# Kernel optimization log

Hardware: AMD Instinct MI355X
Metric: run time of the kernel (lower is better)

Reference implementation:

```python
import jax, jax.numpy as jnp
import numpy as np

N = 100000
E = 1600000
IN_DIM = 128
HID_DIM = 128
OUT_DIM = 128


def _sage_conv(x, src, dst, W_l, b_l, W_r, num_nodes):
    """PyG SAGEConv with mean aggregation:
       out = mean_{j in N(i)} x_j @ W_l + b_l + x_i @ W_r
    edge_index convention: messages flow src -> dst."""
    msg = x[src]                                        # [E, d_in] gather
    agg_sum = jax.ops.segment_sum(msg, dst, num_segments=num_nodes)   # [N, d_in]
    cnt = jax.ops.segment_sum(jnp.ones((msg.shape[0],), x.dtype), dst,
                              num_segments=num_nodes)   # [N]
    agg = agg_sum / jnp.maximum(cnt, 1.0)[:, None]      # scatter-mean (0 for isolated nodes)
    return agg @ W_l + b_l + x @ W_r


def setup_inputs() -> dict:
    key = jax.random.key(0)
    ks = jax.random.split(key, 8)
    def glorot(k, fan_in, fan_out):
        s = jnp.sqrt(2.0 / (fan_in + fan_out))
        return jax.random.normal(k, (fan_in, fan_out), dtype=jnp.float32) * s
    x = jax.random.normal(ks[0], (N, IN_DIM), dtype=jnp.float32)
    edge_index = jax.random.randint(ks[1], (2, E), 0, N, dtype=jnp.int64)
    return {
        "x": x,
        "edge_index": edge_index,
        "W1_l": glorot(ks[2], IN_DIM, HID_DIM),
        "b1": jnp.zeros((HID_DIM,), jnp.float32),
        "W1_r": glorot(ks[3], IN_DIM, HID_DIM),
        "W2_l": glorot(ks[4], HID_DIM, OUT_DIM),
        "b2": jnp.zeros((OUT_DIM,), jnp.float32),
        "W2_r": glorot(ks[5], HID_DIM, OUT_DIM),
    }


def reference(x, edge_index, W1_l, b1, W1_r, W2_l, b2, W2_r):
    src, dst = edge_index[0], edge_index[1]
    h = _sage_conv(x, src, dst, W1_l, b1, W1_r, N)
    h = jax.nn.relu(h)
    # F.dropout(p=0.5, training=self.training): identity in eval mode
    out = _sage_conv(h, src, dst, W2_l, b2, W2_r, N)
    return out
```

## Files before the change

### kernel.cpp

```cpp
#include <hip/hip_runtime.h>
#include <hip/hip_bf16.h>

#define N_NODES 100000
#define N_EDGES 1600000
#define DIM 128
#define BR 32
#define ESTG 2048
#define NB 782
#define CHUNK 16384

typedef __attribute__((ext_vector_type(8))) short bf16x8;
typedef __attribute__((ext_vector_type(4))) float f32x4;
typedef __attribute__((ext_vector_type(2))) float f32x2;

#define OFF_ROWPTR 0
#define OFF_BCNT   (N_NODES + 4)
#define OFF_BBASE  (OFF_BCNT + NB)
#define OFF_BCUR   (OFF_BBASE + NB)
#define OFF_PAIRS  (OFF_BCUR + NB)
#define OFF_COLSRC (OFF_PAIRS + N_EDGES)
#define OFF_HB     (OFF_COLSRC + N_EDGES)
#define OFF_HF8    (OFF_HB + N_NODES * DIM / 2)
#define OFF_WB     (OFF_HF8 + N_NODES * DIM / 4)

__device__ inline unsigned int f2bf(float f) {
    unsigned int u = __float_as_uint(f);
    return (u + 0x7FFFu + ((u >> 16) & 1u)) >> 16;
}

__global__ __launch_bounds__(256) void conv_pack_kernel(
    const float* __restrict__ x, unsigned char* __restrict__ xf8,
    const float* __restrict__ W1l, const float* __restrict__ W1r,
    const float* __restrict__ W2l, const float* __restrict__ W2r,
    unsigned short* __restrict__ WB)
{
    const int b = blockIdx.x;
    const int tid = threadIdx.x;
    if (b < 6250) {
        long i = (long)(b * 256 + tid) * 8;
        float4 a = *(const float4*)(x + i);
        float4 c = *(const float4*)(x + i + 4);
        unsigned int w0 = 0, w1 = 0;
        w0 = __builtin_amdgcn_cvt_pk_fp8_f32(a.x, a.y, w0, false);
        w0 = __builtin_amdgcn_cvt_pk_fp8_f32(a.z, a.w, w0, true);
        w1 = __builtin_amdgcn_cvt_pk_fp8_f32(c.x, c.y, w1, false);
        w1 = __builtin_amdgcn_cvt_pk_fp8_f32(c.z, c.w, w1, true);
        uint2 o; o.x = w0; o.y = w1;
        *(uint2*)(xf8 + i) = o;
    } else {
        int t = (b - 6250) * 256 + tid;
        int layer = t >> 15;
        int rest  = t & 32767;
        int half  = rest >> 14;
        int idx   = rest & 16383;
        int k = idx >> 7;
        int n = idx & 127;
        const float* W = layer ? (half ? W2r : W2l) : (half ? W1r : W1l);
        int kk = half * 128 + k;
        WB[layer * 32768 + (((kk >> 3) * 128 + n) << 3) + (kk & 7)] =
            (unsigned short)f2bf(W[idx]);
    }
}

__global__ __launch_bounds__(256) void bhist_kernel(
    const int* __restrict__ dst, int* __restrict__ bcnt)
{
    __shared__ int histL[NB];
    const int tid = threadIdx.x;
    const int e0 = blockIdx.x * CHUNK;
    const int e1 = min(e0 + CHUNK, N_EDGES);
    for (int b = tid; b < NB; b += 256) histL[b] = 0;
    __syncthreads();
    for (int i = e0 + tid; i < e1; i += 256)
        atomicAdd(&histL[dst[i] >> 7], 1);
    __syncthreads();
    for (int b = tid; b < NB; b += 256) {
        int c = histL[b];
        if (c) atomicAdd(&bcnt[b], c);
    }
}

__global__ __launch_bounds__(1024) void bscan_kernel(
    const int* __restrict__ bcnt, int* __restrict__ bbase,
    int* __restrict__ bcur, int* __restrict__ rowptr)
{
    __shared__ int tmp[1024];
    int tid = threadIdx.x;
    int v = (tid < NB) ? bcnt[tid] : 0;
    tmp[tid] = v;
    __syncthreads();
    for (int off = 1; off < 1024; off <<= 1) {
        int t = (tid >= off) ? tmp[tid - off] : 0;
        __syncthreads();
        tmp[tid] += t;
        __syncthreads();
    }
    if (tid < NB) { int b = tmp[tid] - v; bbase[tid] = b; bcur[tid] = b; }
    if (tid == 0) rowptr[N_NODES] = N_EDGES;
}

__global__ __launch_bounds__(256) void bfill_kernel(
    const int* __restrict__ src, const int* __restrict__ dst,
    int* __restrict__ bcur, unsigned int* __restrict__ pairs)
{
    __shared__ int histL[NB];
    __shared__ int baseL[NB];
    const int tid = threadIdx.x;
    const int e0 = blockIdx.x * CHUNK;
    const int e1 = min(e0 + CHUNK, N_EDGES);
    for (int b = tid; b < NB; b += 256) histL[b] = 0;
    __syncthreads();
    for (int i = e0 + tid; i < e1; i += 256)
        atomicAdd(&histL[dst[i] >> 7], 1);
    __syncthreads();
    for (int b = tid; b < NB; b += 256) {
        int c = histL[b];
        baseL[b] = c ? atomicAdd(&bcur[b], c) : 0;
        histL[b] = 0;
    }
    __syncthreads();
    for (int i = e0 + tid; i < e1; i += 256) {
        int s = src[i];
        int d = dst[i];
        int bk = d >> 7;
        int r = atomicAdd(&histL[bk], 1);
        pairs[baseL[bk] + r] = (unsigned int)s | ((unsigned int)(d & 127) << 25);
    }
}

__global__ __launch_bounds__(256) void bucket_csr_kernel(
    const unsigned int* __restrict__ pairs,
    const int* __restrict__ bcnt, const int* __restrict__ bbase,
    int* __restrict__ rowptr, int* __restrict__ colsrc)
{
    __shared__ int histA[128], exclS[128], hist2[128];
    const int bucket = blockIdx.x;
    const int tid = threadIdx.x;
    const int cnt  = bcnt[bucket];
    const int base = bbase[bucket];
    if (tid < 128) { histA[tid] = 0; hist2[tid] = 0; }
    __syncthreads();
    for (int i = tid; i < cnt; i += 256)
        atomicAdd(&histA[pairs[base + i] >> 25], 1);
    __syncthreads();
    int v = 0;
    if (tid < 128) { v = histA[tid]; exclS[tid] = v; }
    __syncthreads();
    for (int off = 1; off < 128; off <<= 1) {
        int t = 0;
        if (tid < 128 && tid >= off) t = exclS[tid - off];
        __syncthreads();
        if (tid < 128) exclS[tid] += t;
        __syncthreads();
    }
    if (tid < 128) exclS[tid] -= v;
    const int node0 = bucket * 128;
    if (tid < 128 && node0 + tid < N_NODES)
        rowptr[node0 + tid] = base + exclS[tid];
    __syncthreads();
    for (int i = tid; i < cnt; i += 256) {
        unsigned int p = pairs[base + i];
        int dl = (int)(p >> 25);
        int r = atomicAdd(&hist2[dl], 1);
        colsrc[base + exclS[dl] + r] = (int)(p & 0x1FFFFFFu);
    }
}

__device__ inline void addfp8(float* acc, uint2 v) {
    f32x2 p;
    p = __builtin_amdgcn_cvt_pk_f32_fp8((int)v.x, false); acc[0] += p.x; acc[1] += p.y;
    p = __builtin_amdgcn_cvt_pk_f32_fp8((int)v.x, true);  acc[2] += p.x; acc[3] += p.y;
    p = __builtin_amdgcn_cvt_pk_f32_fp8((int)v.y, false); acc[4] += p.x; acc[5] += p.y;
    p = __builtin_amdgcn_cvt_pk_f32_fp8((int)v.y, true);  acc[6] += p.x; acc[7] += p.y;
}

__global__ __launch_bounds__(256, 5) void fused_sage_kernel(
    const unsigned char* __restrict__ f8,
    const float* __restrict__ selfF,
    const unsigned short* __restrict__ selfB,
    const int* __restrict__ rowptr,
    const int* __restrict__ colsrc,
    const unsigned short* __restrict__ WB,
    const float* __restrict__ bias,
    unsigned short* __restrict__ outb,
    unsigned char* __restrict__ outf8,
    float* __restrict__ outf,
    int mode)
{
    __shared__ unsigned short catS[BR * 256];
    __shared__ int eS[ESTG];

    const int tid = threadIdx.x;
    const int block_row = blockIdx.x * BR;
    const int ebase = rowptr[block_row];
    const int span  = rowptr[block_row + BR] - ebase;
    const int smax  = span < ESTG ? span : ESTG;

    for (int i = tid; i < smax; i += 256)
        eS[i] = colsrc[ebase + i] << 7;
    __syncthreads();

    const int c   = tid & 15;
    const int c8  = c * 8;
    const int grp = tid >> 4;

    #pragma unroll
    for (int it = 0; it < 2; ++it) {
        const int nl = grp * 2 + it;
        const int node = block_row + nl;
        const int s  = rowptr[node] - ebase;
        const int e_ = rowptr[node + 1] - ebase;
        const int lim = e_ < ESTG ? e_ : ESTG;

        uint4 sv;
        if (mode) {
            float4 sa = *(const float4*)(selfF + ((long)node << 7) + c8);
            float4 sb = *(const float4*)(selfF + ((long)node << 7) + c8 + 4);
            sv.x = f2bf(sa.x) | (f2bf(sa.y) << 16);
            sv.y = f2bf(sa.z) | (f2bf(sa.w) << 16);
            sv.z = f2bf(sb.x) | (f2bf(sb.y) << 16);
            sv.w = f2bf(sb.z) | (f2bf(sb.w) << 16);
        } else {
            sv = *(const uint4*)(selfB + ((long)node << 7) + c8);
        }

        float acc[8];
        #pragma unroll
        for (int q = 0; q < 8; ++q) acc[q] = 0.0f;

        int i = s;
        for (; i + 8 <= lim; i += 8) {
            const uint2 v0 = *(const uint2*)(f8 + eS[i + 0] + c8);
            const uint2 v1 = *(const uint2*)(f8 + eS[i + 1] + c8);
            const uint2 v2 = *(const uint2*)(f8 + eS[i + 2] + c8);
            const uint2 v3 = *(const uint2*)(f8 + eS[i + 3] + c8);
            const uint2 v4 = *(const uint2*)(f8 + eS[i + 4] + c8);
            const uint2 v5 = *(const uint2*)(f8 + eS[i + 5] + c8);
            const uint2 v6 = *(const uint2*)(f8 + eS[i + 6] + c8);
            const uint2 v7 = *(const uint2*)(f8 + eS[i + 7] + c8);
            addfp8(acc, v0); addfp8(acc, v1); addfp8(acc, v2); addfp8(acc, v3);
            addfp8(acc, v4); addfp8(acc, v5); addfp8(acc, v6); addfp8(acc, v7);
        }
        for (; i < lim; ++i) {
            const uint2 v = *(const uint2*)(f8 + eS[i] + c8);
            addfp8(acc, v);
        }
        for (; i < e_; ++i) {
            const uint2 v = *(const uint2*)(f8 + ((long)colsrc[ebase + i] << 7) + c8);
            addfp8(acc, v);
        }

        const float inv = 1.0f / fmaxf((float)(e_ - s), 1.0f);
        uint4 pv;
        pv.x = f2bf(acc[0] * inv) | (f2bf(acc[1] * inv) << 16);
        pv.y = f2bf(acc[2] * inv) | (f2bf(acc[3] * inv) << 16);
        pv.z = f2bf(acc[4] * inv) | (f2bf(acc[5] * inv) << 16);
        pv.w = f2bf(acc[6] * inv) | (f2bf(acc[7] * inv) << 16);
        const int sw = c ^ (nl & 7);
        *(uint4*)&catS[nl * 256 + sw * 8] = pv;
        *(uint4*)&catS[nl * 256 + 128 + sw * 8] = sv;
    }
    __syncthreads();

    const int w    = tid >> 6;
    const int l    = tid & 63;
    const int wm   = w & 1;
    const int wn   = w >> 1;
    const int lrow = l & 15;
    const int kgrp = l >> 4;
    const int ar   = wm * 16 + lrow;

    f32x4 acc4[4];
    #pragma unroll
    for (int t = 0; t < 4; ++t) acc4[t] = (f32x4){0.f, 0.f, 0.f, 0.f};

    #pragma unroll
    for (int step = 0; step < 8; ++step) {
        const int slot = step * 4 + kgrp;
        bf16x8 a = *(const bf16x8*)&catS[ar * 256 + ((slot ^ (ar & 7)) << 3)];
        #pragma unroll
        for (int t = 0; t < 4; ++t) {
            const int n = wn * 64 + t * 16 + lrow;
            bf16x8 b = *(const bf16x8*)(WB + ((slot * 128 + n) << 3));
            acc4[t] = __builtin_amdgcn_mfma_f32_16x16x32_bf16(a, b, acc4[t], 0, 0, 0);
        }
    }

    const long orow0 = block_row + wm * 16 + kgrp * 4;
    const int  cbase = wn * 64 + lrow;
    #pragma unroll
    for (int t = 0; t < 4; ++t) {
        const int col = cbase + t * 16;
        const float bb = bias[col];
        #pragma unroll
        for (int j = 0; j < 4; ++j) {
            float v = acc4[t][j] + bb;
            const long row = orow0 + j;
            if (mode) {
                v = fmaxf(v, 0.0f);
                outb[row * DIM + col] = (unsigned short)f2bf(v);
                outf8[row * DIM + col] =
                    (unsigned char)(__builtin_amdgcn_cvt_pk_fp8_f32(v, v, 0u, false) & 0xFFu);
            } else {
                outf[row * DIM + col] = v;
            }
        }
    }
}

extern "C" void kernel_launch(void* const* d_in, const int* in_sizes, int n_in,
                              void* d_out, int out_size, void* d_ws, size_t ws_size,
                              hipStream_t stream)
{
    const float* x   = (const float*)d_in[0];
    const int*   ei  = (const int*)d_in[1];
    const float* W1l = (const float*)d_in[2];
    const float* b1  = (const float*)d_in[3];
    const float* W1r = (const float*)d_in[4];
    const float* W2l = (const float*)d_in[5];
    const float* b2  = (const float*)d_in[6];
    const float* W2r = (const float*)d_in[7];
    float* out = (float*)d_out;

    const int* src = ei;
    const int* dst = ei + N_EDGES;

    int* wsi = (int*)d_ws;
    int* rowptr = wsi + OFF_ROWPTR;
    int* bcnt   = wsi + OFF_BCNT;
    int* bbase  = wsi + OFF_BBASE;
    int* bcur   = wsi + OFF_BCUR;
    unsigned int* pairs = (unsigned int*)(wsi + OFF_PAIRS);
    int* colsrc = wsi + OFF_COLSRC;
    unsigned short* hb  = (unsigned short*)(wsi + OFF_HB);
    unsigned char*  hf8 = (unsigned char*)(wsi + OFF_HF8);
    unsigned short* WB  = (unsigned short*)(wsi + OFF_WB);

    unsigned char* xf8 = (unsigned char*)d_out;

    hipMemsetAsync(bcnt, 0, (size_t)NB * sizeof(int), stream);

    conv_pack_kernel<<<6506, 256, 0, stream>>>(x, xf8, W1l, W1r, W2l, W2r, WB);

    const int eblocks = (N_EDGES + CHUNK - 1) / CHUNK;
    bhist_kernel<<<eblocks, 256, 0, stream>>>(dst, bcnt);
    bscan_kernel<<<1, 1024, 0, stream>>>(bcnt, bbase, bcur, rowptr);
    bfill_kernel<<<eblocks, 256, 0, stream>>>(src, dst, bcur, pairs);
    bucket_csr_kernel<<<NB, 256, 0, stream>>>(pairs, bcnt, bbase, rowptr, colsrc);

    const int gblocks = N_NODES / BR;
    fused_sage_kernel<<<gblocks, 256, 0, stream>>>(
        xf8, x, (const unsigned short*)nullptr, rowptr, colsrc,
        WB, b1, hb, hf8, (float*)nullptr, 1);
    fused_sage_kernel<<<gblocks, 256, 0, stream>>>(
        hf8, (const float*)nullptr, hb, rowptr, colsrc,
        WB + 32768, b2, (unsigned short*)nullptr, (unsigned char*)nullptr, out, 0);
}
```

Before: 216.7 us.

## Merge histogram into pack kernel, raise occupancy, and unroll gather tail

Folds the bucket-histogram kernel into the conversion/pack kernel as extra blocks, which removes one launch and lets the histogram overlap with the fp8 conversion. The fused SAGE kernel's minimum-waves hint goes from 5 to 8 and the shared edge staging buffer shrinks from 2048 to 1024 entries, aiming for more resident blocks. Edges beyond the stage then fall back to slower global colsrc reads. The scalar remainder loop becomes a 4/2/1 unrolled tail to expose more memory-level parallelism. The higher occupancy target may also force register spills.

```diff
diff --git a/kernel.cpp b/kernel.cpp
--- a/kernel.cpp
+++ b/kernel.cpp
@@ -5,7 +5,7 @@
 #define N_EDGES 1600000
 #define DIM 128
 #define BR 32
-#define ESTG 2048
+#define ESTG 1024
 #define NB 782
 #define CHUNK 16384
 
@@ -32,8 +32,10 @@
     const float* __restrict__ x, unsigned char* __restrict__ xf8,
     const float* __restrict__ W1l, const float* __restrict__ W1r,
     const float* __restrict__ W2l, const float* __restrict__ W2r,
-    unsigned short* __restrict__ WB)
-{
+    unsigned short* __restrict__ WB,
+    const int* __restrict__ dst, int* __restrict__ bcnt)
+{
+    __shared__ int histL[NB];
     const int b = blockIdx.x;
     const int tid = threadIdx.x;
     if (b < 6250) {
@@ -47,7 +49,7 @@
         w1 = __builtin_amdgcn_cvt_pk_fp8_f32(c.z, c.w, w1, true);
         uint2 o; o.x = w0; o.y = w1;
         *(uint2*)(xf8 + i) = o;
-    } else {
+    } else if (b < 6506) {
         int t = (b - 6250) * 256 + tid;
         int layer = t >> 15;
         int rest  = t & 32767;
@@ -59,24 +61,18 @@
         int kk = half * 128 + k;
         WB[layer * 32768 + (((kk >> 3) * 128 + n) << 3) + (kk & 7)] =
             (unsigned short)f2bf(W[idx]);
-    }
-}
-
-__global__ __launch_bounds__(256) void bhist_kernel(
-    const int* __restrict__ dst, int* __restrict__ bcnt)
-{
-    __shared__ int histL[NB];
-    const int tid = threadIdx.x;
-    const int e0 = blockIdx.x * CHUNK;
-    const int e1 = min(e0 + CHUNK, N_EDGES);
-    for (int b = tid; b < NB; b += 256) histL[b] = 0;
-    __syncthreads();
-    for (int i = e0 + tid; i < e1; i += 256)
-        atomicAdd(&histL[dst[i] >> 7], 1);
-    __syncthreads();
-    for (int b = tid; b < NB; b += 256) {
-        int c = histL[b];
-        if (c) atomicAdd(&bcnt[b], c);
+    } else {
+        const int e0 = (b - 6506) * CHUNK;
+        const int e1 = min(e0 + CHUNK, N_EDGES);
+        for (int q = tid; q < NB; q += 256) histL[q] = 0;
+        __syncthreads();
+        for (int i = e0 + tid; i < e1; i += 256)
+            atomicAdd(&histL[dst[i] >> 7], 1);
+        __syncthreads();
+        for (int q = tid; q < NB; q += 256) {
+            int c = histL[q];
+            if (c) atomicAdd(&bcnt[q], c);
+        }
     }
 }
 
@@ -174,7 +170,7 @@
     p = __builtin_amdgcn_cvt_pk_f32_fp8((int)v.y, true);  acc[6] += p.x; acc[7] += p.y;
 }
 
-__global__ __launch_bounds__(256, 5) void fused_sage_kernel(
+__global__ __launch_bounds__(256, 8) void fused_sage_kernel(
     const unsigned char* __restrict__ f8,
     const float* __restrict__ selfF,
     const unsigned short* __restrict__ selfB,
@@ -241,9 +237,24 @@
             addfp8(acc, v0); addfp8(acc, v1); addfp8(acc, v2); addfp8(acc, v3);
             addfp8(acc, v4); addfp8(acc, v5); addfp8(acc, v6); addfp8(acc, v7);
         }
-        for (; i < lim; ++i) {
+        if (i + 4 <= lim) {
+            const uint2 v0 = *(const uint2*)(f8 + eS[i + 0] + c8);
+            const uint2 v1 = *(const uint2*)(f8 + eS[i + 1] + c8);
+            const uint2 v2 = *(const uint2*)(f8 + eS[i + 2] + c8);
+            const uint2 v3 = *(const uint2*)(f8 + eS[i + 3] + c8);
+            addfp8(acc, v0); addfp8(acc, v1); addfp8(acc, v2); addfp8(acc, v3);
+            i += 4;
+        }
+        if (i + 2 <= lim) {
+            const uint2 v0 = *(const uint2*)(f8 + eS[i + 0] + c8);
+            const uint2 v1 = *(const uint2*)(f8 + eS[i + 1] + c8);
+            addfp8(acc, v0); addfp8(acc, v1);
+            i += 2;
+        }
+        if (i < lim) {
             const uint2 v = *(const uint2*)(f8 + eS[i] + c8);
             addfp8(acc, v);
+            ++i;
         }
         for (; i < e_; ++i) {
             const uint2 v = *(const uint2*)(f8 + ((long)colsrc[ebase + i] << 7) + c8);
@@ -340,10 +351,9 @@
 
     hipMemsetAsync(bcnt, 0, (size_t)NB * sizeof(int), stream);
 
-    conv_pack_kernel<<<6506, 256, 0, stream>>>(x, xf8, W1l, W1r, W2l, W2r, WB);
-
     const int eblocks = (N_EDGES + CHUNK - 1) / CHUNK;
-    bhist_kernel<<<eblocks, 256, 0, stream>>>(dst, bcnt);
+    conv_pack_kernel<<<6506 + eblocks, 256, 0, stream>>>(
+        x, xf8, W1l, W1r, W2l, W2r, WB, dst, bcnt);
     bscan_kernel<<<1, 1024, 0, stream>>>(bcnt, bbase, bcur, rowptr);
     bfill_kernel<<<eblocks, 256, 0, stream>>>(src, dst, bcur, pairs);
     bucket_csr_kernel<<<NB, 256, 0, stream>>>(pairs, bcnt, bbase, rowptr, colsrc);
```

Result: no change. 220.8 us (+1.9%).
